# Kernel optimization log

Measured on AMD Instinct MI355X. Metric: run time of the kernel, lower is better.

Reference implementation:

```python
import jax, jax.numpy as jnp
import numpy as np

N_FFT = 512
HOP = 128
WIN = 512
BATCH = 32
N_SAMPLES = 480000


def make_forward_basis():
    n_freq = N_FFT // 2 + 1  # 257
    # periodic hann window (torch.hann_window default periodic=True)
    n = np.arange(WIN, dtype=np.float32)
    window = 0.5 * (1.0 - np.cos(2.0 * np.pi * n / WIN))
    freqs = np.linspace(0.0, N_FFT // 2, n_freq, dtype=np.float32)  # [n_freq]
    t = np.arange(WIN, dtype=np.float32)
    phase = 2.0 * np.pi * freqs[:, None] * t[None, :] / N_FFT
    real = np.cos(phase) * window[None, :]
    imag = -np.sin(phase) * window[None, :]
    basis = np.concatenate([real, imag], axis=0)[:, None, :]
    return jnp.asarray(basis, dtype=jnp.float32)


def setup_inputs() -> dict:
    key = jax.random.key(0)
    x = jax.random.normal(key, (BATCH, N_SAMPLES), dtype=jnp.float32)
    return {"x": x, "forward_basis": make_forward_basis()}


def reference(x, forward_basis):
    # x: [B, T] -> [B, 1, T]
    x = x[:, None, :]
    pad = N_FFT // 2
    x_padded = jnp.pad(x, ((0, 0), (0, 0), (pad, pad)), mode="reflect")
    # single conv over concatenated real+imag basis: [B, 2*n_freq, n_frames]
    spec = jax.lax.conv_general_dilated(
        x_padded, forward_basis,
        window_strides=(HOP,), padding="VALID",
        dimension_numbers=("NCH", "OIH", "NCH"))
    n_freq = N_FFT // 2 + 1
    real_spec = spec[:, :n_freq, :]
    imag_spec = spec[:, n_freq:, :]
    return jnp.sqrt(real_spec ** 2 + imag_spec ** 2)
```

## Files before the change

### kernel.cpp

```cpp
#include <hip/hip_runtime.h>

#define NFREQ   257
#define NFRAMES 3751
#define NS      480000
#define HOP     128
#define WIN     512

#define NB      32
#define BN      128
#define NFT     30
#define STEPS   32

#define XWPITCH 272
#define XWROWS  131
#define XW_B    35632
#define AHALF   16384
#define WNYQ_B  1024

typedef __attribute__((ext_vector_type(8))) short short8;
typedef __attribute__((ext_vector_type(4))) float f32x4;

__device__ __forceinline__ short f2bf(float f) {
    __bf16 b = (__bf16)f;
    return __builtin_bit_cast(short, b);
}

__device__ __forceinline__ float bf2f(short s) {
    unsigned int u = ((unsigned int)(unsigned short)s) << 16;
    return __builtin_bit_cast(float, u);
}

__device__ __forceinline__ void gload_lds16(const void* g, void* l) {
    __builtin_amdgcn_global_load_lds(
        (const __attribute__((address_space(1))) void*)g,
        (__attribute__((address_space(3))) void*)l,
        16, 0, 0);
}

__global__ __launch_bounds__(256)
void prep_basis2(const float* __restrict__ basis,
                 short* __restrict__ abL, short* __restrict__ wnyqG) {
    int g = blockIdx.x * 256 + threadIdx.x;
    if (g < 32768) {
        int ob   = g * 16;
        int s    = ob >> 14;
        int rem  = ob & 16383;
        int c    = rem >> 10;
        int lane = (rem >> 4) & 63;
        int r    = (c & 7) * 8 + (lane >> 3);
        int plane = (c >> 3) & 1;
        int fr   = (s >> 3) * 64 + r;
        int kel  = (((s & 7) * 128 + 16 * ((lane & 7) ^ (r & 7))) >> 1);
        const float4* p = reinterpret_cast<const float4*>(
            basis + ((size_t)(plane * NFREQ + fr)) * WIN + kel);
        float4 a0 = p[0], a1 = p[1];
        short8 v;
        v[0]=f2bf(a0.x); v[1]=f2bf(a0.y); v[2]=f2bf(a0.z); v[3]=f2bf(a0.w);
        v[4]=f2bf(a1.x); v[5]=f2bf(a1.y); v[6]=f2bf(a1.z); v[7]=f2bf(a1.w);
        *reinterpret_cast<short8*>(reinterpret_cast<char*>(abL) + ob) = v;
    } else if (g < 32832) {
        int j = g - 32768;
        const float4* p = reinterpret_cast<const float4*>(
            basis + (size_t)256 * WIN + j * 8);
        float4 a0 = p[0], a1 = p[1];
        short8 v;
        v[0]=f2bf(a0.x); v[1]=f2bf(a0.y); v[2]=f2bf(a0.z); v[3]=f2bf(a0.w);
        v[4]=f2bf(a1.x); v[5]=f2bf(a1.y); v[6]=f2bf(a1.z); v[7]=f2bf(a1.w);
        *reinterpret_cast<short8*>(wnyqG + j * 8) = v;
    }
}

__global__ __launch_bounds__(256, 2)
void stft_mfma_kernel(const float* __restrict__ x,
                      const short* __restrict__ abL,
                      const short* __restrict__ wnyqG,
                      float* __restrict__ out)
{
    __shared__ __align__(16) char smem[XW_B + 2 * AHALF + WNYQ_B];
    char* const xw   = smem;
    char* const aBuf = smem + XW_B;
    char* const wnyq = smem + XW_B + 2 * AHALF;

    const int tid  = threadIdx.x;
    const int wave = tid >> 6;
    const int lane = tid & 63;
    const int wr   = wave >> 1;
    const int wc   = wave & 1;
    const int lgrp = lane >> 4;
    const int l15  = lane & 15;

    const int logical = (blockIdx.x & 7) * 120 + (blockIdx.x >> 3);
    const int ft = logical % NFT;
    const int b  = logical / NFT;
    const int t0 = ft * BN;

    const char* abLc = (const char*)abL;

    #pragma unroll
    for (int i = 0; i < 4; ++i) {
        int c = wave * 4 + i;
        gload_lds16(abLc + c * 1024 + lane * 16,
                    aBuf + ((c & 8) ? 8192 : 0) + (c & 7) * 1024);
    }
    if (wave == 0)
        gload_lds16((const char*)wnyqG + lane * 16, wnyq);

    {
        const float* __restrict__ xb = x + (size_t)b * NS;
        const int sbase = t0 * 128 - 256;
        #pragma unroll
        for (int i = 0; i < 9; ++i) {
            int g = tid + i * 256;
            if (g < 2096) {
                int ix = sbase + g * 8;
                short8 v;
                if (ix >= 0 && ix + 8 <= NS) {
                    const float4* p = reinterpret_cast<const float4*>(xb + ix);
                    float4 a0 = p[0], a1 = p[1];
                    v[0]=f2bf(a0.x); v[1]=f2bf(a0.y); v[2]=f2bf(a0.z); v[3]=f2bf(a0.w);
                    v[4]=f2bf(a1.x); v[5]=f2bf(a1.y); v[6]=f2bf(a1.z); v[7]=f2bf(a1.w);
                } else {
                    #pragma unroll
                    for (int q = 0; q < 8; ++q) {
                        int idx = ix + q;
                        if (idx < 0) idx = -idx;
                        if (idx >= NS + 256) { v[q] = 0; continue; }
                        if (idx >= NS) idx = 2 * NS - 2 - idx;
                        v[q] = f2bf(xb[idx]);
                    }
                }
                *reinterpret_cast<short8*>(xw + (g >> 4) * XWPITCH + (g & 15) * 16) = v;
            }
        }
    }

    f32x4 accR[2][4], accI[2][4];
    #pragma unroll
    for (int m = 0; m < 2; ++m)
        #pragma unroll
        for (int nt = 0; nt < 4; ++nt) {
            accR[m][nt] = f32x4{0.f, 0.f, 0.f, 0.f};
            accI[m][nt] = f32x4{0.f, 0.f, 0.f, 0.f};
        }

    const int tlb = (wc * 64 + l15) * XWPITCH;

    #pragma unroll 1
    for (int s = 0; s < STEPS; ++s) {
        asm volatile("s_waitcnt vmcnt(0)" ::: "memory");
        __builtin_amdgcn_sched_barrier(0);
        __syncthreads();
        __builtin_amdgcn_sched_barrier(0);

        char* const aCur = aBuf + (s & 1) * AHALF;

        if (s + 1 < STEPS) {
            char* const aNxt = aBuf + ((s + 1) & 1) * AHALF;
            const char* sb = abLc + (size_t)(s + 1) * 16384;
            #pragma unroll
            for (int i = 0; i < 4; ++i) {
                int c = wave * 4 + i;
                gload_lds16(sb + c * 1024 + lane * 16,
                            aNxt + ((c & 8) ? 8192 : 0) + (c & 7) * 1024);
            }
        }
        __builtin_amdgcn_sched_barrier(0);

        const int ksb2 = (s & 7) * 128;
        #pragma unroll
        for (int ko = 0; ko < 2; ++ko) {
            const int kb = ko * 64 + lgrp * 16;
            short8 aRv[2], aIv[2], xv[4];
            #pragma unroll
            for (int m = 0; m < 2; ++m) {
                int row = wr * 32 + m * 16 + l15;
                int o = row * 128 + (kb ^ ((row & 7) << 4));
                aRv[m] = *reinterpret_cast<const short8*>(aCur + o);
                aIv[m] = *reinterpret_cast<const short8*>(aCur + 8192 + o);
            }
            {
                int r8 = ksb2 + kb;
                int T  = r8 + ((r8 >> 4) & 0x30);
                #pragma unroll
                for (int nt = 0; nt < 4; ++nt)
                    xv[nt] = *reinterpret_cast<const short8*>(xw + tlb + nt * (16 * XWPITCH) + T);
            }
            #pragma unroll
            for (int m = 0; m < 2; ++m)
                #pragma unroll
                for (int nt = 0; nt < 4; ++nt) {
                    accR[m][nt] = __builtin_amdgcn_mfma_f32_16x16x32_bf16(aRv[m], xv[nt], accR[m][nt], 0, 0, 0);
                    accI[m][nt] = __builtin_amdgcn_mfma_f32_16x16x32_bf16(aIv[m], xv[nt], accI[m][nt], 0, 0, 0);
                }
        }

        if ((s & 7) == 7) {
            const int fq = s >> 3;
            const int fBase = fq * 64 + wr * 32 + lgrp * 4;
            const int tBase = t0 + wc * 64 + l15;
            float* ob = out + (size_t)b * NFREQ * NFRAMES;
            #pragma unroll
            for (int m = 0; m < 2; ++m)
                #pragma unroll
                for (int nt = 0; nt < 4; ++nt) {
                    int t = tBase + nt * 16;
                    if (t < NFRAMES) {
                        #pragma unroll
                        for (int r = 0; r < 4; ++r) {
                            int f = fBase + m * 16 + r;
                            float vr = accR[m][nt][r], vi = accI[m][nt][r];
                            ob[(size_t)f * NFRAMES + t] = sqrtf(vr * vr + vi * vi);
                        }
                    }
                    accR[m][nt] = f32x4{0.f, 0.f, 0.f, 0.f};
                    accI[m][nt] = f32x4{0.f, 0.f, 0.f, 0.f};
                }
        }
    }

    {
        const int fl = wave * 32 + (lane & 31);
        const int h  = lane >> 5;
        const int xbase = (fl + 2 * h) * XWPITCH;
        const int wbase = h * 512;
        float acc = 0.f;
        #pragma unroll
        for (int j = 0; j < 32; ++j) {
            short8 xv8 = *reinterpret_cast<const short8*>(
                xw + xbase + (j >> 4) * XWPITCH + (j & 15) * 16);
            short8 wv8 = *reinterpret_cast<const short8*>(wnyq + wbase + j * 16);
            #pragma unroll
            for (int q = 0; q < 8; ++q)
                acc = fmaf(bf2f(xv8[q]), bf2f(wv8[q]), acc);
        }
        acc += __shfl_xor(acc, 32);
        int t = t0 + fl;
        if (h == 0 && t < NFRAMES)
            out[((size_t)b * NFREQ + 256) * NFRAMES + t] = fabsf(acc);
    }
}

extern "C" void kernel_launch(void* const* d_in, const int* in_sizes, int n_in,
                              void* d_out, int out_size, void* d_ws, size_t ws_size,
                              hipStream_t stream) {
    const float* x     = (const float*)d_in[0];
    const float* basis = (const float*)d_in[1];
    float* out = (float*)d_out;

    short* abL   = (short*)d_ws;
    short* wnyqG = abL + 262144;

    prep_basis2<<<dim3(129), 256, 0, stream>>>(basis, abL, wnyqG);
    stft_mfma_kernel<<<dim3(NFT * NB), 256, 0, stream>>>(x, abL, wnyqG, out);
}
```

Measured before the change: 88.50 us.

## Double block tile to 256 frames × 128 freqs with 8 waves

Enlarges each workgroup's tile from 128 frames and 64 frequency rows per step to 256 frames and 128 frequency rows, using 512 threads (8 waves) and 4x4 accumulator tiles per wave. The basis layout from the prep kernel is reorganized to match the larger per-step chunk. The goal is more reuse of each loaded basis chunk and signal window, with fewer redundant overlap loads and fewer blocks. The cost is about 136KB of LDS per block and more accumulator registers, which lowers occupancy. There are also only 480 blocks, which may leave CUs unevenly loaded.

Measured after the change: 92.62 us. 1.05x slower.

```diff
diff --git a/kernel.cpp b/kernel.cpp
--- a/kernel.cpp
+++ b/kernel.cpp
@@ -7,15 +7,16 @@
 #define WIN     512
 
 #define NB      32
-#define BN      128
-#define NFT     30
-#define STEPS   32
+#define BN      256
+#define NFT     15
+#define STEPS   16
 
 #define XWPITCH 272
-#define XWROWS  131
-#define XW_B    35632
-#define AHALF   16384
+#define XWROWS  259
+#define XW_B    70448
+#define AHALF   32768
 #define WNYQ_B  1024
+#define XGROUPS 4144
 
 typedef __attribute__((ext_vector_type(8))) short short8;
 typedef __attribute__((ext_vector_type(4))) float f32x4;
@@ -42,22 +43,20 @@
                  short* __restrict__ abL, short* __restrict__ wnyqG) {
     int g = blockIdx.x * 256 + threadIdx.x;
     if (g < 32768) {
-        int ob   = g * 16;
-        int s    = ob >> 14;
-        int rem  = ob & 16383;
-        int c    = rem >> 10;
-        int lane = (rem >> 4) & 63;
-        int r    = (c & 7) * 8 + (lane >> 3);
-        int plane = (c >> 3) & 1;
-        int fr   = (s >> 3) * 64 + r;
-        int kel  = (((s & 7) * 128 + 16 * ((lane & 7) ^ (r & 7))) >> 1);
+        int s    = g >> 11;
+        int c    = g & 2047;
+        int plane = c >> 10;
+        int r    = (c >> 3) & 127;
+        int colg = c & 7;
+        int fr   = (s >> 3) * 128 + r;
+        int kel  = (((s & 7) * 128 + ((colg * 16) ^ ((r & 7) << 4))) >> 1);
         const float4* p = reinterpret_cast<const float4*>(
             basis + ((size_t)(plane * NFREQ + fr)) * WIN + kel);
         float4 a0 = p[0], a1 = p[1];
         short8 v;
         v[0]=f2bf(a0.x); v[1]=f2bf(a0.y); v[2]=f2bf(a0.z); v[3]=f2bf(a0.w);
         v[4]=f2bf(a1.x); v[5]=f2bf(a1.y); v[6]=f2bf(a1.z); v[7]=f2bf(a1.w);
-        *reinterpret_cast<short8*>(reinterpret_cast<char*>(abL) + ob) = v;
+        *reinterpret_cast<short8*>(reinterpret_cast<char*>(abL) + (size_t)g * 16) = v;
     } else if (g < 32832) {
         int j = g - 32768;
         const float4* p = reinterpret_cast<const float4*>(
@@ -70,7 +69,7 @@
     }
 }
 
-__global__ __launch_bounds__(256, 2)
+__global__ __launch_bounds__(512, 2)
 void stft_mfma_kernel(const float* __restrict__ x,
                       const short* __restrict__ abL,
                       const short* __restrict__ wnyqG,
@@ -84,12 +83,12 @@
     const int tid  = threadIdx.x;
     const int wave = tid >> 6;
     const int lane = tid & 63;
-    const int wr   = wave >> 1;
-    const int wc   = wave & 1;
+    const int wr   = wave >> 2;
+    const int wc   = wave & 3;
     const int lgrp = lane >> 4;
     const int l15  = lane & 15;
 
-    const int logical = (blockIdx.x & 7) * 120 + (blockIdx.x >> 3);
+    const int logical = (blockIdx.x & 7) * 60 + (blockIdx.x >> 3);
     const int ft = logical % NFT;
     const int b  = logical / NFT;
     const int t0 = ft * BN;
@@ -98,9 +97,8 @@
 
     #pragma unroll
     for (int i = 0; i < 4; ++i) {
-        int c = wave * 4 + i;
-        gload_lds16(abLc + c * 1024 + lane * 16,
-                    aBuf + ((c & 8) ? 8192 : 0) + (c & 7) * 1024);
+        int c = wave * 256 + i * 64 + lane;
+        gload_lds16(abLc + (size_t)c * 16, aBuf + c * 16);
     }
     if (wave == 0)
         gload_lds16((const char*)wnyqG + lane * 16, wnyq);
@@ -110,8 +108,8 @@
         const int sbase = t0 * 128 - 256;
         #pragma unroll
         for (int i = 0; i < 9; ++i) {
-            int g = tid + i * 256;
-            if (g < 2096) {
+            int g = tid + i * 512;
+            if (g < XGROUPS) {
                 int ix = sbase + g * 8;
                 short8 v;
                 if (ix >= 0 && ix + 8 <= NS) {
@@ -134,9 +132,9 @@
         }
     }
 
-    f32x4 accR[2][4], accI[2][4];
+    f32x4 accR[4][4], accI[4][4];
     #pragma unroll
-    for (int m = 0; m < 2; ++m)
+    for (int m = 0; m < 4; ++m)
         #pragma unroll
         for (int nt = 0; nt < 4; ++nt) {
             accR[m][nt] = f32x4{0.f, 0.f, 0.f, 0.f};
@@ -156,12 +154,11 @@
 
         if (s + 1 < STEPS) {
             char* const aNxt = aBuf + ((s + 1) & 1) * AHALF;
-            const char* sb = abLc + (size_t)(s + 1) * 16384;
+            const char* sb = abLc + (size_t)(s + 1) * 32768;
             #pragma unroll
             for (int i = 0; i < 4; ++i) {
-                int c = wave * 4 + i;
-                gload_lds16(sb + c * 1024 + lane * 16,
-                            aNxt + ((c & 8) ? 8192 : 0) + (c & 7) * 1024);
+                int c = wave * 256 + i * 64 + lane;
+                gload_lds16(sb + (size_t)c * 16, aNxt + c * 16);
             }
         }
         __builtin_amdgcn_sched_barrier(0);
@@ -170,13 +167,13 @@
         #pragma unroll
         for (int ko = 0; ko < 2; ++ko) {
             const int kb = ko * 64 + lgrp * 16;
-            short8 aRv[2], aIv[2], xv[4];
-            #pragma unroll
-            for (int m = 0; m < 2; ++m) {
-                int row = wr * 32 + m * 16 + l15;
+            short8 aRv[4], aIv[4], xv[4];
+            #pragma unroll
+            for (int m = 0; m < 4; ++m) {
+                int row = wr * 64 + m * 16 + l15;
                 int o = row * 128 + (kb ^ ((row & 7) << 4));
                 aRv[m] = *reinterpret_cast<const short8*>(aCur + o);
-                aIv[m] = *reinterpret_cast<const short8*>(aCur + 8192 + o);
+                aIv[m] = *reinterpret_cast<const short8*>(aCur + 16384 + o);
             }
             {
                 int r8 = ksb2 + kb;
@@ -186,7 +183,7 @@
                     xv[nt] = *reinterpret_cast<const short8*>(xw + tlb + nt * (16 * XWPITCH) + T);
             }
             #pragma unroll
-            for (int m = 0; m < 2; ++m)
+            for (int m = 0; m < 4; ++m)
                 #pragma unroll
                 for (int nt = 0; nt < 4; ++nt) {
                     accR[m][nt] = __builtin_amdgcn_mfma_f32_16x16x32_bf16(aRv[m], xv[nt], accR[m][nt], 0, 0, 0);
@@ -195,12 +192,12 @@
         }
 
         if ((s & 7) == 7) {
-            const int fq = s >> 3;
-            const int fBase = fq * 64 + wr * 32 + lgrp * 4;
+            const int fp = s >> 3;
+            const int fBase = fp * 128 + wr * 64 + lgrp * 4;
             const int tBase = t0 + wc * 64 + l15;
             float* ob = out + (size_t)b * NFREQ * NFRAMES;
             #pragma unroll
-            for (int m = 0; m < 2; ++m)
+            for (int m = 0; m < 4; ++m)
                 #pragma unroll
                 for (int nt = 0; nt < 4; ++nt) {
                     int t = tBase + nt * 16;
@@ -251,5 +248,5 @@
     short* wnyqG = abL + 262144;
 
     prep_basis2<<<dim3(129), 256, 0, stream>>>(basis, abL, wnyqG);
-    stft_mfma_kernel<<<dim3(NFT * NB), 256, 0, stream>>>(x, abL, wnyqG, out);
-}
+    stft_mfma_kernel<<<dim3(NFT * NB), 512, 0, stream>>>(x, abL, wnyqG, out);
+}
```

## Load basis fragments directly from global into registers, drop LDS staging

Applied to the files above, without the earlier changes.

The basis matrix is now stored in plain row-major bf16. Each wave reads its own A fragments straight from global memory (L2-resident) into registers, with a two-stage register prefetch, so the double-buffered LDS copy of the basis and the per-step barriers go away. The wave tiling changes from a 2x2 grid of 64x64 tiles to four waves each covering 32 frequencies across all 128 frames, which doubles the accumulators per wave. This cuts LDS footprint and synchronisation, but adds global-load latency to the inner loop and raises register pressure, which may hurt occupancy.

Result: slower. 102.9 us (+16.3%).

```diff
diff --git a/kernel.cpp b/kernel.cpp
--- a/kernel.cpp
+++ b/kernel.cpp
@@ -9,12 +9,9 @@
 #define NB      32
 #define BN      128
 #define NFT     30
-#define STEPS   32
-
+#define NH      32
 #define XWPITCH 272
-#define XWROWS  131
 #define XW_B    35632
-#define AHALF   16384
 #define WNYQ_B  1024
 
 typedef __attribute__((ext_vector_type(8))) short short8;
@@ -24,44 +21,35 @@
     __bf16 b = (__bf16)f;
     return __builtin_bit_cast(short, b);
 }
-
 __device__ __forceinline__ float bf2f(short s) {
     unsigned int u = ((unsigned int)(unsigned short)s) << 16;
     return __builtin_bit_cast(float, u);
 }
-
 __device__ __forceinline__ void gload_lds16(const void* g, void* l) {
     __builtin_amdgcn_global_load_lds(
         (const __attribute__((address_space(1))) void*)g,
-        (__attribute__((address_space(3))) void*)l,
-        16, 0, 0);
+        (__attribute__((address_space(3))) void*)l, 16, 0, 0);
 }
 
 __global__ __launch_bounds__(256)
-void prep_basis2(const float* __restrict__ basis,
-                 short* __restrict__ abL, short* __restrict__ wnyqG) {
+void prep_basis3(const float* __restrict__ basis,
+                 short* __restrict__ abf, short* __restrict__ wnyqG) {
     int g = blockIdx.x * 256 + threadIdx.x;
     if (g < 32768) {
-        int ob   = g * 16;
-        int s    = ob >> 14;
-        int rem  = ob & 16383;
-        int c    = rem >> 10;
-        int lane = (rem >> 4) & 63;
-        int r    = (c & 7) * 8 + (lane >> 3);
-        int plane = (c >> 3) & 1;
-        int fr   = (s >> 3) * 64 + r;
-        int kel  = (((s & 7) * 128 + 16 * ((lane & 7) ^ (r & 7))) >> 1);
+        int plane = g >> 14;
+        int rem   = g & 16383;
+        int row   = rem >> 6;
+        int kg    = rem & 63;
         const float4* p = reinterpret_cast<const float4*>(
-            basis + ((size_t)(plane * NFREQ + fr)) * WIN + kel);
+            basis + ((size_t)(plane * NFREQ + row)) * WIN + kg * 8);
         float4 a0 = p[0], a1 = p[1];
         short8 v;
         v[0]=f2bf(a0.x); v[1]=f2bf(a0.y); v[2]=f2bf(a0.z); v[3]=f2bf(a0.w);
         v[4]=f2bf(a1.x); v[5]=f2bf(a1.y); v[6]=f2bf(a1.z); v[7]=f2bf(a1.w);
-        *reinterpret_cast<short8*>(reinterpret_cast<char*>(abL) + ob) = v;
+        *reinterpret_cast<short8*>(abf + ((size_t)(plane * 256 + row)) * WIN + kg * 8) = v;
     } else if (g < 32832) {
         int j = g - 32768;
-        const float4* p = reinterpret_cast<const float4*>(
-            basis + (size_t)256 * WIN + j * 8);
+        const float4* p = reinterpret_cast<const float4*>(basis + (size_t)256 * WIN + j * 8);
         float4 a0 = p[0], a1 = p[1];
         short8 v;
         v[0]=f2bf(a0.x); v[1]=f2bf(a0.y); v[2]=f2bf(a0.z); v[3]=f2bf(a0.w);
@@ -72,20 +60,17 @@
 
 __global__ __launch_bounds__(256, 2)
 void stft_mfma_kernel(const float* __restrict__ x,
-                      const short* __restrict__ abL,
+                      const short* __restrict__ abf,
                       const short* __restrict__ wnyqG,
                       float* __restrict__ out)
 {
-    __shared__ __align__(16) char smem[XW_B + 2 * AHALF + WNYQ_B];
+    __shared__ __align__(16) char smem[XW_B + WNYQ_B];
     char* const xw   = smem;
-    char* const aBuf = smem + XW_B;
-    char* const wnyq = smem + XW_B + 2 * AHALF;
+    char* const wnyq = smem + XW_B;
 
     const int tid  = threadIdx.x;
     const int wave = tid >> 6;
     const int lane = tid & 63;
-    const int wr   = wave >> 1;
-    const int wc   = wave & 1;
     const int lgrp = lane >> 4;
     const int l15  = lane & 15;
 
@@ -94,14 +79,6 @@
     const int b  = logical / NFT;
     const int t0 = ft * BN;
 
-    const char* abLc = (const char*)abL;
-
-    #pragma unroll
-    for (int i = 0; i < 4; ++i) {
-        int c = wave * 4 + i;
-        gload_lds16(abLc + c * 1024 + lane * 16,
-                    aBuf + ((c & 8) ? 8192 : 0) + (c & 7) * 1024);
-    }
     if (wave == 0)
         gload_lds16((const char*)wnyqG + lane * 16, wnyq);
 
@@ -133,87 +110,94 @@
             }
         }
     }
-
-    f32x4 accR[2][4], accI[2][4];
+    __syncthreads();
+
+    const char* const aB = (const char*)abf + wave * 32768 + l15 * 1024 + lgrp * 16;
+
+    f32x4 accR[2][8], accI[2][8];
     #pragma unroll
     for (int m = 0; m < 2; ++m)
         #pragma unroll
-        for (int nt = 0; nt < 4; ++nt) {
-            accR[m][nt] = f32x4{0.f, 0.f, 0.f, 0.f};
-            accI[m][nt] = f32x4{0.f, 0.f, 0.f, 0.f};
-        }
-
-    const int tlb = (wc * 64 + l15) * XWPITCH;
+        for (int n = 0; n < 8; ++n) {
+            accR[m][n] = f32x4{0.f,0.f,0.f,0.f};
+            accI[m][n] = f32x4{0.f,0.f,0.f,0.f};
+        }
+
+    short8 R0[2], I0[2], R1[2], I1[2];
+
+    #define AOFF(h) ((((h) >> 4) << 17) + ((((h) >> 1) & 7) << 7) + (((h) & 1) << 6))
+
+    #pragma unroll
+    for (int m = 0; m < 2; ++m) {
+        R0[m] = *reinterpret_cast<const short8*>(aB + m * 16384);
+        I0[m] = *reinterpret_cast<const short8*>(aB + 262144 + m * 16384);
+    }
+
+    #define COMPUTE(h, R, I)                                                        \
+    {                                                                               \
+        int r8 = ((((h) >> 1) & 7) << 7) + (((h) & 1) << 6) + lgrp * 16;            \
+        int T  = r8 + ((r8 >> 4) & 0x30);                                           \
+        const char* xwl = xw + l15 * XWPITCH + T;                                   \
+        _Pragma("unroll")                                                           \
+        for (int nh = 0; nh < 2; ++nh) {                                            \
+            short8 xv[4];                                                           \
+            _Pragma("unroll")                                                       \
+            for (int j = 0; j < 4; ++j)                                             \
+                xv[j] = *reinterpret_cast<const short8*>(                           \
+                    xwl + (nh * 4 + j) * (16 * XWPITCH));                           \
+            _Pragma("unroll")                                                       \
+            for (int m = 0; m < 2; ++m)                                             \
+                _Pragma("unroll")                                                   \
+                for (int j = 0; j < 4; ++j) {                                       \
+                    accR[m][nh*4+j] = __builtin_amdgcn_mfma_f32_16x16x32_bf16(      \
+                        (R)[m], xv[j], accR[m][nh*4+j], 0, 0, 0);                   \
+                    accI[m][nh*4+j] = __builtin_amdgcn_mfma_f32_16x16x32_bf16(      \
+                        (I)[m], xv[j], accI[m][nh*4+j], 0, 0, 0);                   \
+                }                                                                   \
+        }                                                                           \
+    }
 
     #pragma unroll 1
-    for (int s = 0; s < STEPS; ++s) {
-        asm volatile("s_waitcnt vmcnt(0)" ::: "memory");
-        __builtin_amdgcn_sched_barrier(0);
-        __syncthreads();
-        __builtin_amdgcn_sched_barrier(0);
-
-        char* const aCur = aBuf + (s & 1) * AHALF;
-
-        if (s + 1 < STEPS) {
-            char* const aNxt = aBuf + ((s + 1) & 1) * AHALF;
-            const char* sb = abLc + (size_t)(s + 1) * 16384;
-            #pragma unroll
-            for (int i = 0; i < 4; ++i) {
-                int c = wave * 4 + i;
-                gload_lds16(sb + c * 1024 + lane * 16,
-                            aNxt + ((c & 8) ? 8192 : 0) + (c & 7) * 1024);
+    for (int hh = 0; hh < NH; hh += 2) {
+        {
+            const int boff = AOFF(hh + 1);
+            #pragma unroll
+            for (int m = 0; m < 2; ++m) {
+                R1[m] = *reinterpret_cast<const short8*>(aB + boff + m * 16384);
+                I1[m] = *reinterpret_cast<const short8*>(aB + boff + 262144 + m * 16384);
             }
         }
-        __builtin_amdgcn_sched_barrier(0);
-
-        const int ksb2 = (s & 7) * 128;
-        #pragma unroll
-        for (int ko = 0; ko < 2; ++ko) {
-            const int kb = ko * 64 + lgrp * 16;
-            short8 aRv[2], aIv[2], xv[4];
+        COMPUTE(hh, R0, I0);
+        if (hh + 2 < NH) {
+            const int boff = AOFF(hh + 2);
             #pragma unroll
             for (int m = 0; m < 2; ++m) {
-                int row = wr * 32 + m * 16 + l15;
-                int o = row * 128 + (kb ^ ((row & 7) << 4));
-                aRv[m] = *reinterpret_cast<const short8*>(aCur + o);
-                aIv[m] = *reinterpret_cast<const short8*>(aCur + 8192 + o);
+                R0[m] = *reinterpret_cast<const short8*>(aB + boff + m * 16384);
+                I0[m] = *reinterpret_cast<const short8*>(aB + boff + 262144 + m * 16384);
             }
-            {
-                int r8 = ksb2 + kb;
-                int T  = r8 + ((r8 >> 4) & 0x30);
-                #pragma unroll
-                for (int nt = 0; nt < 4; ++nt)
-                    xv[nt] = *reinterpret_cast<const short8*>(xw + tlb + nt * (16 * XWPITCH) + T);
-            }
+        }
+        COMPUTE(hh + 1, R1, I1);
+
+        if ((hh & 15) == 14) {
+            const int fp = hh >> 4;
+            float* ob = out + (size_t)b * NFREQ * NFRAMES;
+            const int fb = fp * 128 + wave * 32 + lgrp * 4;
+            const int tb = t0 + l15;
             #pragma unroll
             for (int m = 0; m < 2; ++m)
                 #pragma unroll
-                for (int nt = 0; nt < 4; ++nt) {
-                    accR[m][nt] = __builtin_amdgcn_mfma_f32_16x16x32_bf16(aRv[m], xv[nt], accR[m][nt], 0, 0, 0);
-                    accI[m][nt] = __builtin_amdgcn_mfma_f32_16x16x32_bf16(aIv[m], xv[nt], accI[m][nt], 0, 0, 0);
-                }
-        }
-
-        if ((s & 7) == 7) {
-            const int fq = s >> 3;
-            const int fBase = fq * 64 + wr * 32 + lgrp * 4;
-            const int tBase = t0 + wc * 64 + l15;
-            float* ob = out + (size_t)b * NFREQ * NFRAMES;
-            #pragma unroll
-            for (int m = 0; m < 2; ++m)
-                #pragma unroll
-                for (int nt = 0; nt < 4; ++nt) {
-                    int t = tBase + nt * 16;
+                for (int nt = 0; nt < 8; ++nt) {
+                    int t = tb + nt * 16;
                     if (t < NFRAMES) {
                         #pragma unroll
                         for (int r = 0; r < 4; ++r) {
-                            int f = fBase + m * 16 + r;
+                            int f = fb + m * 16 + r;
                             float vr = accR[m][nt][r], vi = accI[m][nt][r];
                             ob[(size_t)f * NFRAMES + t] = sqrtf(vr * vr + vi * vi);
                         }
                     }
-                    accR[m][nt] = f32x4{0.f, 0.f, 0.f, 0.f};
-                    accI[m][nt] = f32x4{0.f, 0.f, 0.f, 0.f};
+                    accR[m][nt] = f32x4{0.f,0.f,0.f,0.f};
+                    accI[m][nt] = f32x4{0.f,0.f,0.f,0.f};
                 }
         }
     }
@@ -247,9 +231,9 @@
     const float* basis = (const float*)d_in[1];
     float* out = (float*)d_out;
 
-    short* abL   = (short*)d_ws;
-    short* wnyqG = abL + 262144;
-
-    prep_basis2<<<dim3(129), 256, 0, stream>>>(basis, abL, wnyqG);
-    stft_mfma_kernel<<<dim3(NFT * NB), 256, 0, stream>>>(x, abL, wnyqG, out);
-}
+    short* abf   = (short*)d_ws;
+    short* wnyqG = abf + 262144;
+
+    prep_basis3<<<dim3(129), 256, 0, stream>>>(basis, abf, wnyqG);
+    stft_mfma_kernel<<<dim3(NFT * NB), 256, 0, stream>>>(x, abf, wnyqG, out);
+}
```

## Retile STFT MFMA so each wave covers all 128 frames and 32 freqs

Applied to the files above, without the earlier changes.

Changes the per-step tile so each wave computes a 32-frequency by 128-frame block. Each step now covers 128 frequencies and 32 k-values instead of 64 frequencies and 64 k-values, and the basis prep kernel writes the matching swizzled layout. Each A fragment is reused across 8 x fragments, which reduces LDS reads of the basis per MFMA. In exchange the accumulator count doubles to 64 f32x4 registers per thread, which may raise register pressure and lower occupancy below the 2 blocks per CU requested by launch bounds.

New measurement: 87.58 us (median of 2 runs). No clear change (-1.0%).

```diff
diff --git a/kernel.cpp b/kernel.cpp
--- a/kernel.cpp
+++ b/kernel.cpp
@@ -10,12 +10,11 @@
 #define BN      128
 #define NFT     30
 #define STEPS   32
-
 #define XWPITCH 272
-#define XWROWS  131
 #define XW_B    35632
 #define AHALF   16384
 #define WNYQ_B  1024
+#define XGROUPS 2096
 
 typedef __attribute__((ext_vector_type(8))) short short8;
 typedef __attribute__((ext_vector_type(4))) float f32x4;
@@ -24,35 +23,36 @@
     __bf16 b = (__bf16)f;
     return __builtin_bit_cast(short, b);
 }
-
 __device__ __forceinline__ float bf2f(short s) {
     unsigned int u = ((unsigned int)(unsigned short)s) << 16;
     return __builtin_bit_cast(float, u);
 }
-
 __device__ __forceinline__ void gload_lds16(const void* g, void* l) {
     __builtin_amdgcn_global_load_lds(
         (const __attribute__((address_space(1))) void*)g,
-        (__attribute__((address_space(3))) void*)l,
-        16, 0, 0);
+        (__attribute__((address_space(3))) void*)l, 16, 0, 0);
 }
 
 __global__ __launch_bounds__(256)
-void prep_basis2(const float* __restrict__ basis,
+void prep_basis4(const float* __restrict__ basis,
                  short* __restrict__ abL, short* __restrict__ wnyqG) {
     int g = blockIdx.x * 256 + threadIdx.x;
     if (g < 32768) {
         int ob   = g * 16;
-        int s    = ob >> 14;
+        int step = ob >> 14;
         int rem  = ob & 16383;
-        int c    = rem >> 10;
-        int lane = (rem >> 4) & 63;
-        int r    = (c & 7) * 8 + (lane >> 3);
-        int plane = (c >> 3) & 1;
-        int fr   = (s >> 3) * 64 + r;
-        int kel  = (((s & 7) * 128 + 16 * ((lane & 7) ^ (r & 7))) >> 1);
+        int pl   = rem >> 13;
+        int r    = (rem >> 7) & 63;
+        int s    = (rem >> 4) & 7;
+        int u    = s ^ (r & 7);
+        int f    = r + (u >> 2) * 64;
+        int kg   = u & 3;
+        int fp   = step >> 4;
+        int ks32 = step & 15;
+        int row  = pl * NFREQ + fp * 128 + f;
+        int k0   = ks32 * 32 + kg * 8;
         const float4* p = reinterpret_cast<const float4*>(
-            basis + ((size_t)(plane * NFREQ + fr)) * WIN + kel);
+            basis + (size_t)row * WIN + k0);
         float4 a0 = p[0], a1 = p[1];
         short8 v;
         v[0]=f2bf(a0.x); v[1]=f2bf(a0.y); v[2]=f2bf(a0.z); v[3]=f2bf(a0.w);
@@ -60,8 +60,7 @@
         *reinterpret_cast<short8*>(reinterpret_cast<char*>(abL) + ob) = v;
     } else if (g < 32832) {
         int j = g - 32768;
-        const float4* p = reinterpret_cast<const float4*>(
-            basis + (size_t)256 * WIN + j * 8);
+        const float4* p = reinterpret_cast<const float4*>(basis + (size_t)256 * WIN + j * 8);
         float4 a0 = p[0], a1 = p[1];
         short8 v;
         v[0]=f2bf(a0.x); v[1]=f2bf(a0.y); v[2]=f2bf(a0.z); v[3]=f2bf(a0.w);
@@ -84,8 +83,6 @@
     const int tid  = threadIdx.x;
     const int wave = tid >> 6;
     const int lane = tid & 63;
-    const int wr   = wave >> 1;
-    const int wc   = wave & 1;
     const int lgrp = lane >> 4;
     const int l15  = lane & 15;
 
@@ -99,8 +96,7 @@
     #pragma unroll
     for (int i = 0; i < 4; ++i) {
         int c = wave * 4 + i;
-        gload_lds16(abLc + c * 1024 + lane * 16,
-                    aBuf + ((c & 8) ? 8192 : 0) + (c & 7) * 1024);
+        gload_lds16(abLc + c * 1024 + lane * 16, aBuf + c * 1024);
     }
     if (wave == 0)
         gload_lds16((const char*)wnyqG + lane * 16, wnyq);
@@ -111,7 +107,7 @@
         #pragma unroll
         for (int i = 0; i < 9; ++i) {
             int g = tid + i * 256;
-            if (g < 2096) {
+            if (g < XGROUPS) {
                 int ix = sbase + g * 8;
                 short8 v;
                 if (ix >= 0 && ix + 8 <= NS) {
@@ -134,16 +130,17 @@
         }
     }
 
-    f32x4 accR[2][4], accI[2][4];
+    f32x4 accR[2][8], accI[2][8];
     #pragma unroll
     for (int m = 0; m < 2; ++m)
         #pragma unroll
-        for (int nt = 0; nt < 4; ++nt) {
-            accR[m][nt] = f32x4{0.f, 0.f, 0.f, 0.f};
-            accI[m][nt] = f32x4{0.f, 0.f, 0.f, 0.f};
-        }
-
-    const int tlb = (wc * 64 + l15) * XWPITCH;
+        for (int n = 0; n < 8; ++n) {
+            accR[m][n] = f32x4{0.f,0.f,0.f,0.f};
+            accI[m][n] = f32x4{0.f,0.f,0.f,0.f};
+        }
+
+    const int rb = (wave & 1) * 32 + l15;
+    const int ub = (wave >> 1) * 4 + lgrp;
 
     #pragma unroll 1
     for (int s = 0; s < STEPS; ++s) {
@@ -156,64 +153,60 @@
 
         if (s + 1 < STEPS) {
             char* const aNxt = aBuf + ((s + 1) & 1) * AHALF;
-            const char* sb = abLc + (size_t)(s + 1) * 16384;
+            const char* sb = abLc + (size_t)(s + 1) * AHALF;
             #pragma unroll
             for (int i = 0; i < 4; ++i) {
                 int c = wave * 4 + i;
-                gload_lds16(sb + c * 1024 + lane * 16,
-                            aNxt + ((c & 8) ? 8192 : 0) + (c & 7) * 1024);
+                gload_lds16(sb + c * 1024 + lane * 16, aNxt + c * 1024);
             }
         }
         __builtin_amdgcn_sched_barrier(0);
 
-        const int ksb2 = (s & 7) * 128;
-        #pragma unroll
-        for (int ko = 0; ko < 2; ++ko) {
-            const int kb = ko * 64 + lgrp * 16;
-            short8 aRv[2], aIv[2], xv[4];
-            #pragma unroll
-            for (int m = 0; m < 2; ++m) {
-                int row = wr * 32 + m * 16 + l15;
-                int o = row * 128 + (kb ^ ((row & 7) << 4));
-                aRv[m] = *reinterpret_cast<const short8*>(aCur + o);
-                aIv[m] = *reinterpret_cast<const short8*>(aCur + 8192 + o);
+        const int ks32 = s & 15;
+        short8 aRv[2], aIv[2], xv[8];
+        #pragma unroll
+        for (int m = 0; m < 2; ++m) {
+            int r   = rb + m * 16;
+            int off = r * 128 + ((ub ^ (r & 7)) << 4);
+            aRv[m] = *reinterpret_cast<const short8*>(aCur + off);
+            aIv[m] = *reinterpret_cast<const short8*>(aCur + 8192 + off);
+        }
+        {
+            int r8 = ks32 * 64 + lgrp * 16;
+            int T  = r8 + ((r8 >> 8) << 4);
+            const char* xwl = xw + l15 * XWPITCH + T;
+            #pragma unroll
+            for (int nt = 0; nt < 8; ++nt)
+                xv[nt] = *reinterpret_cast<const short8*>(xwl + nt * (16 * XWPITCH));
+        }
+        #pragma unroll
+        for (int m = 0; m < 2; ++m)
+            #pragma unroll
+            for (int nt = 0; nt < 8; ++nt) {
+                accR[m][nt] = __builtin_amdgcn_mfma_f32_16x16x32_bf16(aRv[m], xv[nt], accR[m][nt], 0, 0, 0);
+                accI[m][nt] = __builtin_amdgcn_mfma_f32_16x16x32_bf16(aIv[m], xv[nt], accI[m][nt], 0, 0, 0);
             }
-            {
-                int r8 = ksb2 + kb;
-                int T  = r8 + ((r8 >> 4) & 0x30);
-                #pragma unroll
-                for (int nt = 0; nt < 4; ++nt)
-                    xv[nt] = *reinterpret_cast<const short8*>(xw + tlb + nt * (16 * XWPITCH) + T);
-            }
+
+        if ((s & 15) == 15) {
+            const int fp = s >> 4;
+            float* ob = out + (size_t)b * NFREQ * NFRAMES;
+            const int fb = fp * 128 + wave * 32 + lgrp * 4;
+            const int tb = t0 + l15;
             #pragma unroll
             for (int m = 0; m < 2; ++m)
                 #pragma unroll
-                for (int nt = 0; nt < 4; ++nt) {
-                    accR[m][nt] = __builtin_amdgcn_mfma_f32_16x16x32_bf16(aRv[m], xv[nt], accR[m][nt], 0, 0, 0);
-                    accI[m][nt] = __builtin_amdgcn_mfma_f32_16x16x32_bf16(aIv[m], xv[nt], accI[m][nt], 0, 0, 0);
-                }
-        }
-
-        if ((s & 7) == 7) {
-            const int fq = s >> 3;
-            const int fBase = fq * 64 + wr * 32 + lgrp * 4;
-            const int tBase = t0 + wc * 64 + l15;
-            float* ob = out + (size_t)b * NFREQ * NFRAMES;
-            #pragma unroll
-            for (int m = 0; m < 2; ++m)
-                #pragma unroll
-                for (int nt = 0; nt < 4; ++nt) {
-                    int t = tBase + nt * 16;
+                for (int nt = 0; nt < 8; ++nt) {
+                    int t = tb + nt * 16;
                     if (t < NFRAMES) {
                         #pragma unroll
                         for (int r = 0; r < 4; ++r) {
-                            int f = fBase + m * 16 + r;
+                            int f = fb + m * 16 + r;
                             float vr = accR[m][nt][r], vi = accI[m][nt][r];
                             ob[(size_t)f * NFRAMES + t] = sqrtf(vr * vr + vi * vi);
                         }
                     }
-                    accR[m][nt] = f32x4{0.f, 0.f, 0.f, 0.f};
-                    accI[m][nt] = f32x4{0.f, 0.f, 0.f, 0.f};
+                    accR[m][nt] = f32x4{0.f,0.f,0.f,0.f};
+                    accI[m][nt] = f32x4{0.f,0.f,0.f,0.f};
                 }
         }
     }
@@ -250,6 +243,6 @@
     short* abL   = (short*)d_ws;
     short* wnyqG = abL + 262144;
 
-    prep_basis2<<<dim3(129), 256, 0, stream>>>(basis, abL, wnyqG);
+    prep_basis4<<<dim3(129), 256, 0, stream>>>(basis, abL, wnyqG);
     stft_mfma_kernel<<<dim3(NFT * NB), 256, 0, stream>>>(x, abL, wnyqG, out);
 }
```
